# Optimization experiments

Measured on AMD Instinct MI355X. Metric: run time of the kernel, lower is better.

Reference implementation:

```python
import jax, jax.numpy as jnp
import numpy as np

SEG_LENS = [2048, 8192]
DIL_RATES = [1, 2]


def _dilated_attention(q, k, v, is_causal):
    # q,k,v: [b, n, h, d]
    b, n, h, d = q.shape
    ng = len(SEG_LENS)
    g = h // ng  # heads per group (even split)
    scale = 1.0 / np.sqrt(d).astype(np.float32)
    out = jnp.zeros_like(q)
    for i, (s, r) in enumerate(zip(SEG_LENS, DIL_RATES)):
        hs = i * g
        offset = i % r  # offset_idx % dilation_rate, as in _create_dilation_pattern
        idx = np.arange(offset, s, r)  # dilated positions within a segment, length m
        m = idx.shape[0]
        ns = n // s  # number of segments
        # reshape to segments then gather dilated positions: [b, ns, m, g, d]
        qg = q[:, :, hs:hs + g, :].reshape(b, ns, s, g, d)[:, :, idx]
        kg = k[:, :, hs:hs + g, :].reshape(b, ns, s, g, d)[:, :, idx]
        vg = v[:, :, hs:hs + g, :].reshape(b, ns, s, g, d)[:, :, idx]
        # segment-local attention over dilated tokens only (structured sparsity)
        scores = jnp.einsum('bsqhd,bskhd->bshqk', qg, kg) * scale
        if is_causal:
            cm = np.tril(np.ones((m, m), dtype=bool))  # idx is sorted -> causal in dilated order
            scores = jnp.where(cm, scores, -jnp.inf)
        attn = jax.nn.softmax(scores, axis=-1)
        og = jnp.einsum('bshqk,bskhd->bsqhd', attn, vg)  # [b, ns, m, g, d]
        # scatter back to full segment positions; non-dilated positions stay zero
        full = jnp.zeros((b, ns, s, g, d), q.dtype).at[:, :, idx].set(og)
        out = out.at[:, :, hs:hs + g, :].set(full.reshape(b, n, g, d))
    return out


def setup_inputs() -> dict:
    key = jax.random.key(0)
    k1, k2, k3 = jax.random.split(key, 3)
    shape = (1, 8192, 8, 64)
    q = jax.random.normal(k1, shape, dtype=jnp.float32)
    k = jax.random.normal(k2, shape, dtype=jnp.float32)
    v = jax.random.normal(k3, shape, dtype=jnp.float32)
    return {"q": q, "k": k, "v": v, "is_causal": 1}


def reference(q, k, v, is_causal):
    return _dilated_attention(q, k, v, bool(is_causal))
```

## Files before the change

### kernel.cpp

```cpp
#include <hip/hip_runtime.h>


#define LP 72

typedef __attribute__((ext_vector_type(8))) short bf16x8;
typedef __attribute__((ext_vector_type(4))) float f32x4;
typedef __attribute__((ext_vector_type(4))) unsigned u32x4;
typedef const unsigned int __attribute__((address_space(1)))* gp1;
typedef unsigned int __attribute__((address_space(3)))* lp3;

__device__ __forceinline__ unsigned short f2bf(float f) {
  unsigned u = __builtin_bit_cast(unsigned, f);
  u += 0x7fff + ((u >> 16) & 1);
  return (unsigned short)(u >> 16);
}

__device__ __forceinline__ int region_base(int head) {
  return (head < 4) ? head * 524288 : 2097152 + (head - 4) * 262144;
}

__device__ __forceinline__ void gl_lds16(const unsigned short* g, unsigned short* l) {
  __builtin_amdgcn_global_load_lds((gp1)g, (lp3)l, 16, 0, 0);
}

__global__ __launch_bounds__(256, 4)
void prep_kernel(const float* __restrict__ K, const float* __restrict__ V,
                 unsigned short* __restrict__ Kb, unsigned short* __restrict__ Vt) {
  __shared__ unsigned short sT[64][LP];
  const int bid = blockIdx.x;
  int head, pos0, rate, off;
  if (bid < 512) { head = bid >> 7; pos0 = (bid & 127) * 64; rate = 1; off = 0; }
  else { int b = bid - 512; head = 4 + (b >> 6); pos0 = (b & 63) * 64; rate = 2; off = 1; }
  const int rb = region_base(head);
  const int tid = threadIdx.x;
  const int row = tid >> 2, dg = tid & 3;
  const long tok = (long)(pos0 + row) * rate + off;

  {
    const float* kp = K + tok * 512 + head * 64 + dg * 16;
    unsigned short tmp[16];
    #pragma unroll
    for (int i = 0; i < 4; ++i) {
      float4 f = ((const float4*)kp)[i];
      tmp[i * 4 + 0] = f2bf(f.x); tmp[i * 4 + 1] = f2bf(f.y);
      tmp[i * 4 + 2] = f2bf(f.z); tmp[i * 4 + 3] = f2bf(f.w);
    }
    const int s = row & 7;
    unsigned short* dstrow = Kb + rb + (long)(pos0 + row) * 64;
    *(int4*)(dstrow + (((2 * dg)     ^ s) * 8)) = ((int4*)tmp)[0];
    *(int4*)(dstrow + (((2 * dg + 1) ^ s) * 8)) = ((int4*)tmp)[1];
  }

  {
    const float* vp = V + tok * 512 + head * 64 + dg * 16;
    #pragma unroll
    for (int i = 0; i < 4; ++i) {
      float4 f = ((const float4*)vp)[i];
      unsigned* p = (unsigned*)&sT[row][dg * 16 + i * 4];
      p[0] = (unsigned)f2bf(f.x) | ((unsigned)f2bf(f.y) << 16);
      p[1] = (unsigned)f2bf(f.z) | ((unsigned)f2bf(f.w) << 16);
    }
  }
  __syncthreads();

  {
    const int wv = tid >> 6, lane = tid & 63;
    unsigned pk[8];
    #pragma unroll
    for (int j = 0; j < 8; ++j) {
      unsigned lo = sT[wv * 16 + 2 * j][lane];
      unsigned hi = sT[wv * 16 + 2 * j + 1][lane];
      pk[j] = lo | (hi << 16);
    }
    int4 a = {(int)pk[0], (int)pk[1], (int)pk[2], (int)pk[3]};
    int4 b = {(int)pk[4], (int)pk[5], (int)pk[6], (int)pk[7]};
    const int dt = lane >> 4, l16p = lane & 15, h = wv >> 1;
    const int qa = (wv & 1) * 2, qb = qa + 1;
    unsigned short* dstc = Vt + rb + (long)pos0 * 64;
    *(int4*)(dstc + (dt * 2 + h) * 512 + (qa * 16 + l16p) * 8) = a;
    *(int4*)(dstc + (dt * 2 + h) * 512 + (qb * 16 + l16p) * 8) = b;
  }
}

__global__ __launch_bounds__(256, 2)
void attn_kernel(const float* __restrict__ Q, const unsigned short* __restrict__ Kb,
                 const unsigned short* __restrict__ Vt, const int* __restrict__ IC,
                 float* __restrict__ O, float* __restrict__ Slots) {
  __shared__ __attribute__((aligned(16))) unsigned short sK[2][4096];

  const int bid = blockIdx.x;
  int head, q0, seg0, mseg, rate, off, grp, chunk, slot;
  if (bid < 512) {
    int h4 = bid & 3;
    int u = bid >> 2;
    chunk = u >> 6;
    int t = 63 - (u & 63);
    head = 4 + h4; seg0 = 0; mseg = 4096;
    rate = 2; off = 1; grp = 1;
    q0 = t * 64;
    slot = (h4 * 64 + t) * 2 + chunk;
  } else {
    int cc = bid - 512;
    int job = (cc & 7) | ((cc >> 8) << 3);
    int tloc = (cc & 255) >> 3;
    head = job & 3;
    seg0 = (job >> 2) * 2048;
    q0 = seg0 + tloc * 64; mseg = 2048;
    rate = 1; off = 0; grp = 0; chunk = 0; slot = 0;
  }
  const int rb = region_base(head);
  const bool causal = (*IC) != 0;
  const int tid = threadIdx.x, wave = tid >> 6, lane = tid & 63;
  const int l16 = lane & 15, quad = lane >> 4;
  const int ch0 = ((quad ^ (l16 & 7)) * 8);
  const int ch1 = ch0 ^ 32;

  const int qloc = q0 - seg0;
  const int diagkb = qloc >> 6;
  const int nkb = causal ? diagkb + 1 : (mseg >> 6);
  const int klo = grp ? chunk * 32 : 0;
  const int khi = grp ? min(nkb, klo + 32) : nkb;
  if (klo >= khi) return;

  const float QSCALE = 0.18033688011112042f;
  bf16x8 aQ[2];
  {
    long tok = (long)(q0 + wave * 16 + l16) * rate + off;
    const float* qp = Q + tok * 512 + head * 64 + quad * 8;
    #pragma unroll
    for (int kc = 0; kc < 2; ++kc) {
      float4 f0 = ((const float4*)(qp + kc * 32))[0];
      float4 f1 = ((const float4*)(qp + kc * 32))[1];
      bf16x8 a;
      a[0] = (short)f2bf(f0.x * QSCALE); a[1] = (short)f2bf(f0.y * QSCALE);
      a[2] = (short)f2bf(f0.z * QSCALE); a[3] = (short)f2bf(f0.w * QSCALE);
      a[4] = (short)f2bf(f1.x * QSCALE); a[5] = (short)f2bf(f1.y * QSCALE);
      a[6] = (short)f2bf(f1.z * QSCALE); a[7] = (short)f2bf(f1.w * QSCALE);
      aQ[kc] = a;
    }
  }

  f32x4 oacc[4];
  float lsum = 0.f;
  #pragma unroll
  for (int dt = 0; dt < 4; ++dt) oacc[dt] = (f32x4){0.f, 0.f, 0.f, 0.f};

  const unsigned short* Ksrc = Kb + rb + (long)seg0 * 64;
  const unsigned short* Vsrc = Vt + rb + (long)seg0 * 64;

  const int o0 = wave * 1024;
  const int lo = lane * 8;
  const int qv = qloc + wave * 16 + l16;

  auto stage_k = [&](int x, int sl) {
    const unsigned short* kt = Ksrc + (long)x * 4096;
    gl_lds16(kt + o0 + lo,       &sK[sl][o0]);
    gl_lds16(kt + o0 + 512 + lo, &sK[sl][o0 + 512]);
  };

  struct PB { bf16x8 b0, b1; };
  auto qk_phase = [&](int kb, const unsigned short* kbuf) -> PB {
    f32x4 sc[4];
    #pragma unroll
    for (int c = 0; c < 4; ++c) {
      const unsigned short* krow = &kbuf[(c * 16 + l16) * 64];
      bf16x8 b0 = *(const bf16x8*)(krow + ch0);
      bf16x8 b1 = *(const bf16x8*)(krow + ch1);
      f32x4 z = (f32x4){0.f, 0.f, 0.f, 0.f};
      z = __builtin_amdgcn_mfma_f32_16x16x32_bf16(b0, aQ[0], z, 0, 0, 0);
      z = __builtin_amdgcn_mfma_f32_16x16x32_bf16(b1, aQ[1], z, 0, 0, 0);
      sc[c] = z;
    }

    float p[4][4];
    if (causal && (kb == diagkb)) {
      #pragma unroll
      for (int c = 0; c < 4; ++c)
        #pragma unroll
        for (int r = 0; r < 4; ++r) {
          float e = __builtin_amdgcn_exp2f(sc[c][r]);
          if (kb * 64 + c * 16 + quad * 4 + r > qv) e = 0.f;
          p[c][r] = e;
        }
    } else {
      #pragma unroll
      for (int c = 0; c < 4; ++c)
        #pragma unroll
        for (int r = 0; r < 4; ++r)
          p[c][r] = __builtin_amdgcn_exp2f(sc[c][r]);
    }

    lsum += (((p[0][0] + p[0][1]) + (p[0][2] + p[0][3])) +
             ((p[1][0] + p[1][1]) + (p[1][2] + p[1][3]))) +
            (((p[2][0] + p[2][1]) + (p[2][2] + p[2][3])) +
             ((p[3][0] + p[3][1]) + (p[3][2] + p[3][3])));

    unsigned W00, W01, W10, W11, W20, W21, W30, W31;
    asm("v_cvt_pk_bf16_f32 %0, %1, %2" : "=v"(W00) : "v"(p[0][0]), "v"(p[0][1]));
    asm("v_cvt_pk_bf16_f32 %0, %1, %2" : "=v"(W01) : "v"(p[0][2]), "v"(p[0][3]));
    asm("v_cvt_pk_bf16_f32 %0, %1, %2" : "=v"(W10) : "v"(p[1][0]), "v"(p[1][1]));
    asm("v_cvt_pk_bf16_f32 %0, %1, %2" : "=v"(W11) : "v"(p[1][2]), "v"(p[1][3]));
    asm("v_cvt_pk_bf16_f32 %0, %1, %2" : "=v"(W20) : "v"(p[2][0]), "v"(p[2][1]));
    asm("v_cvt_pk_bf16_f32 %0, %1, %2" : "=v"(W21) : "v"(p[2][2]), "v"(p[2][3]));
    asm("v_cvt_pk_bf16_f32 %0, %1, %2" : "=v"(W30) : "v"(p[3][0]), "v"(p[3][1]));
    asm("v_cvt_pk_bf16_f32 %0, %1, %2" : "=v"(W31) : "v"(p[3][2]), "v"(p[3][3]));

    unsigned R0 = W00, R2 = W10;
    asm("v_permlane32_swap_b32 %0, %1" : "+v"(R0), "+v"(R2));
    asm("v_permlane16_swap_b32 %0, %1" : "+v"(R0), "+v"(R2));
    unsigned R1 = W01, R3 = W11;
    asm("v_permlane32_swap_b32 %0, %1" : "+v"(R1), "+v"(R3));
    asm("v_permlane16_swap_b32 %0, %1" : "+v"(R1), "+v"(R3));
    unsigned R4 = W20, R6 = W30;
    asm("v_permlane32_swap_b32 %0, %1" : "+v"(R4), "+v"(R6));
    asm("v_permlane16_swap_b32 %0, %1" : "+v"(R4), "+v"(R6));
    unsigned R5 = W21, R7 = W31;
    asm("v_permlane32_swap_b32 %0, %1" : "+v"(R5), "+v"(R7));
    asm("v_permlane16_swap_b32 %0, %1" : "+v"(R5), "+v"(R7));
    u32x4 t0 = {R0, R1, R2, R3};
    u32x4 t1 = {R4, R5, R6, R7};
    PB pb;
    pb.b0 = __builtin_bit_cast(bf16x8, t0);
    pb.b1 = __builtin_bit_cast(bf16x8, t1);
    return pb;
  };

  stage_k(klo, 0);

  for (int kb = klo; kb < khi; ++kb) {
    const int cur = (kb - klo) & 1;
    __syncthreads();

    int4 vr[8];
    {
      const int4* vt = (const int4*)(Vsrc + (long)kb * 4096);
      #pragma unroll
      for (int c = 0; c < 8; ++c) vr[c] = vt[c * 64 + lane];
    }
    if (kb + 1 < khi) stage_k(kb + 1, cur ^ 1);

    PB pb = qk_phase(kb, &sK[cur][0]);

    #pragma unroll
    for (int dt = 0; dt < 4; ++dt) {
      bf16x8 v0 = __builtin_bit_cast(bf16x8, vr[dt * 2]);
      bf16x8 v1 = __builtin_bit_cast(bf16x8, vr[dt * 2 + 1]);
      oacc[dt] = __builtin_amdgcn_mfma_f32_16x16x32_bf16(v0, pb.b0, oacc[dt], 0, 0, 0);
      oacc[dt] = __builtin_amdgcn_mfma_f32_16x16x32_bf16(v1, pb.b1, oacc[dt], 0, 0, 0);
    }
  }

  float ltot = lsum;
  ltot += __shfl_xor(ltot, 16);
  ltot += __shfl_xor(ltot, 32);

  if (grp == 1) {
    float* S = Slots + (long)slot * 4160;
    const int qrow = wave * 16 + l16;
    #pragma unroll
    for (int dt = 0; dt < 4; ++dt)
      #pragma unroll
      for (int r = 0; r < 4; ++r)
        S[qrow * 64 + dt * 16 + quad * 4 + r] = oacc[dt][r];
    if (quad == 0) S[4096 + qrow] = ltot;
  } else {
    const int tq = q0 + wave * 16 + l16;
    const float inv = 1.0f / ltot;
    float* dst = O + (long)tq * 512 + head * 64 + quad * 4;
    #pragma unroll
    for (int dt = 0; dt < 4; ++dt)
      #pragma unroll
      for (int r = 0; r < 4; ++r)
        dst[dt * 16 + r] = oacc[dt][r] * inv;
  }
}

__global__ __launch_bounds__(256, 4)
void combine_kernel(const float* __restrict__ Slots, const int* __restrict__ IC,
                    float* __restrict__ O) {
  const int b = blockIdx.x;
  const int h4 = b >> 6, t = b & 63;
  const bool causal = (*IC) != 0;
  const int nkb = causal ? t + 1 : 64;
  const int nc = (nkb > 32) ? 2 : 1;
  const float* s0 = Slots + (long)((h4 * 64 + t) * 2) * 4160;
  const int tid = threadIdx.x;
  const int row = tid >> 2, dq = (tid & 3) * 16;

  float4 acc[4];
  const float4* p0 = (const float4*)(s0 + row * 64 + dq);
  #pragma unroll
  for (int i = 0; i < 4; ++i) acc[i] = p0[i];
  float l = s0[4096 + row];
  if (nc == 2) {
    const float* s1 = s0 + 4160;
    const float4* p1 = (const float4*)(s1 + row * 64 + dq);
    #pragma unroll
    for (int i = 0; i < 4; ++i) {
      float4 v = p1[i];
      acc[i].x += v.x; acc[i].y += v.y; acc[i].z += v.z; acc[i].w += v.w;
    }
    l += s1[4096 + row];
  }
  const float inv = 1.0f / l;
  const long tok = (long)(t * 64 + row) * 2 + 1;
  float* dst = O + tok * 512 + (4 + h4) * 64 + dq;
  #pragma unroll
  for (int i = 0; i < 4; ++i) {
    float4 o = {acc[i].x * inv, acc[i].y * inv, acc[i].z * inv, acc[i].w * inv};
    ((float4*)dst)[i] = o;
  }
  float* dste = O + (tok - 1) * 512 + (4 + h4) * 64 + dq;
  const float4 z = {0.f, 0.f, 0.f, 0.f};
  #pragma unroll
  for (int i = 0; i < 4; ++i) ((float4*)dste)[i] = z;
}

extern "C" void kernel_launch(void* const* d_in, const int* in_sizes, int n_in,
                              void* d_out, int out_size, void* d_ws, size_t ws_size,
                              hipStream_t stream) {
  const float* q = (const float*)d_in[0];
  const float* k = (const float*)d_in[1];
  const float* v = (const float*)d_in[2];
  const int* ic = (const int*)d_in[3];
  unsigned short* Kb = (unsigned short*)d_ws;
  unsigned short* Vt = Kb + 3145728;
  float* Slots = (float*)((char*)d_ws + 12582912);
  prep_kernel<<<dim3(768), dim3(256), 0, stream>>>(k, v, Kb, Vt);
  attn_kernel<<<dim3(1024), dim3(256), 0, stream>>>(q, Kb, Vt, ic, (float*)d_out, Slots);
  combine_kernel<<<dim3(256), dim3(256), 0, stream>>>(Slots, ic, (float*)d_out);
}
```

Baseline: 128.3 us.

## Split KV range into 16-block chunks for both head groups and interleave blocks

Attention work is now split along the key dimension into chunks of at most 16 key blocks for both the dilated and the dense head groups, so there are 2048 attention blocks instead of 1024. Even and odd block ids alternate between the two groups. Chunk 0 writes its unnormalized partial straight into the output plus a row-sum array. Later chunks write to slots, and a generalized combine kernel adds them and normalizes. Tiles that fit in a single chunk finish directly in the attention kernel. The aim is better load balance and shorter critical paths under causal masking, at the cost of more partial-result traffic and a larger combine pass.

```diff
diff --git a/kernel.cpp b/kernel.cpp
--- a/kernel.cpp
+++ b/kernel.cpp
@@ -85,28 +85,29 @@
 __global__ __launch_bounds__(256, 2)
 void attn_kernel(const float* __restrict__ Q, const unsigned short* __restrict__ Kb,
                  const unsigned short* __restrict__ Vt, const int* __restrict__ IC,
-                 float* __restrict__ O, float* __restrict__ Slots) {
+                 float* __restrict__ O, float* __restrict__ Slots,
+                 float* __restrict__ Lar) {
   __shared__ __attribute__((aligned(16))) unsigned short sK[2][4096];
 
   const int bid = blockIdx.x;
-  int head, q0, seg0, mseg, rate, off, grp, chunk, slot;
-  if (bid < 512) {
-    int h4 = bid & 3;
-    int u = bid >> 2;
-    chunk = u >> 6;
-    int t = 63 - (u & 63);
-    head = 4 + h4; seg0 = 0; mseg = 4096;
-    rate = 2; off = 1; grp = 1;
-    q0 = t * 64;
-    slot = (h4 * 64 + t) * 2 + chunk;
+  int head, q0, seg0, mseg, rate, off, grp, cnk, tloc, tileId;
+  if ((bid & 1) == 0) {
+    int idx = bid >> 1;
+    tloc = 63 - (idx >> 4);
+    cnk  = (idx >> 2) & 3;
+    int h4 = idx & 3;
+    head = 4 + h4; seg0 = 0; mseg = 4096; rate = 2; off = 1; grp = 1;
+    q0 = tloc * 64;
+    tileId = h4 * 64 + tloc;
   } else {
-    int cc = bid - 512;
-    int job = (cc & 7) | ((cc >> 8) << 3);
-    int tloc = (cc & 255) >> 3;
-    head = job & 3;
-    seg0 = (job >> 2) * 2048;
-    q0 = seg0 + tloc * 64; mseg = 2048;
-    rate = 1; off = 0; grp = 0; chunk = 0; slot = 0;
+    int idx = bid >> 1;
+    tloc = 31 - (idx >> 5);
+    cnk  = (idx >> 4) & 1;
+    int hs = idx & 15;
+    head = hs & 3; seg0 = (hs >> 2) * 2048;
+    mseg = 2048; rate = 1; off = 0; grp = 0;
+    q0 = seg0 + tloc * 64;
+    tileId = 256 + hs * 32 + tloc;
   }
   const int rb = region_base(head);
   const bool causal = (*IC) != 0;
@@ -118,9 +119,10 @@
   const int qloc = q0 - seg0;
   const int diagkb = qloc >> 6;
   const int nkb = causal ? diagkb + 1 : (mseg >> 6);
-  const int klo = grp ? chunk * 32 : 0;
-  const int khi = grp ? min(nkb, klo + 32) : nkb;
+  const int klo = cnk * 16;
+  const int khi = min(nkb, klo + 16);
   if (klo >= khi) return;
+  const int ncnk = (nkb + 15) >> 4;
 
   const float QSCALE = 0.18033688011112042f;
   bf16x8 aQ[2];
@@ -254,66 +256,103 @@
   ltot += __shfl_xor(ltot, 16);
   ltot += __shfl_xor(ltot, 32);
 
-  if (grp == 1) {
-    float* S = Slots + (long)slot * 4160;
-    const int qrow = wave * 16 + l16;
+  const int qrow = wave * 16 + l16;
+  if (ncnk == 1) {
+    const int tq = q0 + qrow;
+    const long tok = (long)tq * rate + off;
+    const float inv = 1.0f / ltot;
+    float* dst = O + tok * 512 + head * 64 + quad * 4;
+    #pragma unroll
+    for (int dt = 0; dt < 4; ++dt)
+      #pragma unroll
+      for (int r = 0; r < 4; ++r)
+        dst[dt * 16 + r] = oacc[dt][r] * inv;
+    if (grp) {
+      float* dste = O + (tok - 1) * 512 + head * 64 + quad * 4;
+      #pragma unroll
+      for (int dt = 0; dt < 4; ++dt)
+        #pragma unroll
+        for (int r = 0; r < 4; ++r)
+          dste[dt * 16 + r] = 0.f;
+    }
+  } else if (cnk == 0) {
+    const int tq = q0 + qrow;
+    const long tok = (long)tq * rate + off;
+    float* dst = O + tok * 512 + head * 64 + quad * 4;
+    #pragma unroll
+    for (int dt = 0; dt < 4; ++dt)
+      #pragma unroll
+      for (int r = 0; r < 4; ++r)
+        dst[dt * 16 + r] = oacc[dt][r];
+    if (quad == 0) Lar[tileId * 64 + qrow] = ltot;
+  } else {
+    const int slotId = grp ? (tileId * 3 + (cnk - 1)) : (tileId + 512);
+    float* S = Slots + (long)slotId * 4160;
     #pragma unroll
     for (int dt = 0; dt < 4; ++dt)
       #pragma unroll
       for (int r = 0; r < 4; ++r)
         S[qrow * 64 + dt * 16 + quad * 4 + r] = oacc[dt][r];
     if (quad == 0) S[4096 + qrow] = ltot;
+  }
+}
+
+__global__ __launch_bounds__(256, 4)
+void combine_kernel(const float* __restrict__ Slots, const float* __restrict__ Lar,
+                    const int* __restrict__ IC, float* __restrict__ O) {
+  const int b = blockIdx.x;
+  const bool causal = (*IC) != 0;
+  int grp, head, tloc, tileId, nkb;
+  int seg0 = 0;
+  if (b < 256) {
+    grp = 1; head = 4 + (b & 3); tloc = b >> 2;
+    tileId = (b & 3) * 64 + tloc;
+    nkb = causal ? tloc + 1 : 64;
   } else {
-    const int tq = q0 + wave * 16 + l16;
-    const float inv = 1.0f / ltot;
-    float* dst = O + (long)tq * 512 + head * 64 + quad * 4;
-    #pragma unroll
-    for (int dt = 0; dt < 4; ++dt)
-      #pragma unroll
-      for (int r = 0; r < 4; ++r)
-        dst[dt * 16 + r] = oacc[dt][r] * inv;
-  }
-}
-
-__global__ __launch_bounds__(256, 4)
-void combine_kernel(const float* __restrict__ Slots, const int* __restrict__ IC,
-                    float* __restrict__ O) {
-  const int b = blockIdx.x;
-  const int h4 = b >> 6, t = b & 63;
-  const bool causal = (*IC) != 0;
-  const int nkb = causal ? t + 1 : 64;
-  const int nc = (nkb > 32) ? 2 : 1;
-  const float* s0 = Slots + (long)((h4 * 64 + t) * 2) * 4160;
+    int u = b - 256;
+    grp = 0; int hs = u & 15; head = hs & 3; seg0 = (hs >> 2) * 2048;
+    tloc = u >> 4;
+    tileId = 256 + hs * 32 + tloc;
+    nkb = causal ? tloc + 1 : 32;
+  }
+  const int ncnk = (nkb + 15) >> 4;
+  if (ncnk < 2) return;
+
   const int tid = threadIdx.x;
   const int row = tid >> 2, dq = (tid & 3) * 16;
+  long tok;
+  if (grp) tok = (long)(tloc * 64 + row) * 2 + 1;
+  else     tok = (long)(seg0 + tloc * 64 + row);
+  float* dst = O + tok * 512 + head * 64 + dq;
 
   float4 acc[4];
-  const float4* p0 = (const float4*)(s0 + row * 64 + dq);
   #pragma unroll
-  for (int i = 0; i < 4; ++i) acc[i] = p0[i];
-  float l = s0[4096 + row];
-  if (nc == 2) {
-    const float* s1 = s0 + 4160;
-    const float4* p1 = (const float4*)(s1 + row * 64 + dq);
+  for (int i = 0; i < 4; ++i) acc[i] = ((const float4*)dst)[i];
+  float l = Lar[tileId * 64 + row];
+
+  for (int c = 1; c < ncnk; ++c) {
+    const int slotId = grp ? (tileId * 3 + (c - 1)) : (tileId + 512);
+    const float* S = Slots + (long)slotId * 4160;
+    const float4* p = (const float4*)(S + row * 64 + dq);
     #pragma unroll
     for (int i = 0; i < 4; ++i) {
-      float4 v = p1[i];
+      float4 v = p[i];
       acc[i].x += v.x; acc[i].y += v.y; acc[i].z += v.z; acc[i].w += v.w;
     }
-    l += s1[4096 + row];
+    l += S[4096 + row];
   }
   const float inv = 1.0f / l;
-  const long tok = (long)(t * 64 + row) * 2 + 1;
-  float* dst = O + tok * 512 + (4 + h4) * 64 + dq;
   #pragma unroll
   for (int i = 0; i < 4; ++i) {
     float4 o = {acc[i].x * inv, acc[i].y * inv, acc[i].z * inv, acc[i].w * inv};
     ((float4*)dst)[i] = o;
   }
-  float* dste = O + (tok - 1) * 512 + (4 + h4) * 64 + dq;
-  const float4 z = {0.f, 0.f, 0.f, 0.f};
-  #pragma unroll
-  for (int i = 0; i < 4; ++i) ((float4*)dste)[i] = z;
+  if (grp) {
+    float* dste = O + (tok - 1) * 512 + head * 64 + dq;
+    const float4 z = {0.f, 0.f, 0.f, 0.f};
+    #pragma unroll
+    for (int i = 0; i < 4; ++i) ((float4*)dste)[i] = z;
+  }
 }
 
 extern "C" void kernel_launch(void* const* d_in, const int* in_sizes, int n_in,
@@ -326,7 +365,8 @@
   unsigned short* Kb = (unsigned short*)d_ws;
   unsigned short* Vt = Kb + 3145728;
   float* Slots = (float*)((char*)d_ws + 12582912);
+  float* Lar = Slots + (long)1280 * 4160;
   prep_kernel<<<dim3(768), dim3(256), 0, stream>>>(k, v, Kb, Vt);
-  attn_kernel<<<dim3(1024), dim3(256), 0, stream>>>(q, Kb, Vt, ic, (float*)d_out, Slots);
-  combine_kernel<<<dim3(256), dim3(256), 0, stream>>>(Slots, ic, (float*)d_out);
-}
+  attn_kernel<<<dim3(2048), dim3(256), 0, stream>>>(q, Kb, Vt, ic, (float*)d_out, Slots, Lar);
+  combine_kernel<<<dim3(768), dim3(256), 0, stream>>>(Slots, Lar, ic, (float*)d_out);
+}
```

Measured after the change: 145.1 us. +13.1%, slower.

## Store K in MFMA fragment order and load directly to registers, drop LDS staging

Applied to the files above, without the earlier changes.

The prep kernel now writes K in the same fragment-major layout already used for V, so each lane's MFMA operand sits in contiguous 16-byte chunks. The attention kernel drops the double-buffered LDS staging of K, its global_load_lds calls and the per-iteration __syncthreads, and instead loads K and V straight from global memory into registers. This removes block-wide barriers and LDS traffic. In exchange each wave now fetches K itself with no prefetch of the next block, so load latency is less hidden, and register pressure rises.

```diff
diff --git a/kernel.cpp b/kernel.cpp
--- a/kernel.cpp
+++ b/kernel.cpp
@@ -6,8 +6,6 @@
 typedef __attribute__((ext_vector_type(8))) short bf16x8;
 typedef __attribute__((ext_vector_type(4))) float f32x4;
 typedef __attribute__((ext_vector_type(4))) unsigned u32x4;
-typedef const unsigned int __attribute__((address_space(1)))* gp1;
-typedef unsigned int __attribute__((address_space(3)))* lp3;
 
 __device__ __forceinline__ unsigned short f2bf(float f) {
   unsigned u = __builtin_bit_cast(unsigned, f);
@@ -17,10 +15,6 @@
 
 __device__ __forceinline__ int region_base(int head) {
   return (head < 4) ? head * 524288 : 2097152 + (head - 4) * 262144;
-}
-
-__device__ __forceinline__ void gl_lds16(const unsigned short* g, unsigned short* l) {
-  __builtin_amdgcn_global_load_lds((gp1)g, (lp3)l, 16, 0, 0);
 }
 
 __global__ __launch_bounds__(256, 4)
@@ -45,10 +39,11 @@
       tmp[i * 4 + 0] = f2bf(f.x); tmp[i * 4 + 1] = f2bf(f.y);
       tmp[i * 4 + 2] = f2bf(f.z); tmp[i * 4 + 3] = f2bf(f.w);
     }
-    const int s = row & 7;
-    unsigned short* dstrow = Kb + rb + (long)(pos0 + row) * 64;
-    *(int4*)(dstrow + (((2 * dg)     ^ s) * 8)) = ((int4*)tmp)[0];
-    *(int4*)(dstrow + (((2 * dg + 1) ^ s) * 8)) = ((int4*)tmp)[1];
+    const int c2 = (row >> 4) * 2 + (dg >> 1);
+    const int qp = (dg & 1) * 2;
+    unsigned short* dstc = Kb + rb + (long)pos0 * 64;
+    *(int4*)(dstc + c2 * 512 + ((qp    ) * 16 + (row & 15)) * 8) = ((int4*)tmp)[0];
+    *(int4*)(dstc + c2 * 512 + ((qp + 1) * 16 + (row & 15)) * 8) = ((int4*)tmp)[1];
   }
 
   {
@@ -86,8 +81,6 @@
 void attn_kernel(const float* __restrict__ Q, const unsigned short* __restrict__ Kb,
                  const unsigned short* __restrict__ Vt, const int* __restrict__ IC,
                  float* __restrict__ O, float* __restrict__ Slots) {
-  __shared__ __attribute__((aligned(16))) unsigned short sK[2][4096];
-
   const int bid = blockIdx.x;
   int head, q0, seg0, mseg, rate, off, grp, chunk, slot;
   if (bid < 512) {
@@ -112,8 +105,6 @@
   const bool causal = (*IC) != 0;
   const int tid = threadIdx.x, wave = tid >> 6, lane = tid & 63;
   const int l16 = lane & 15, quad = lane >> 4;
-  const int ch0 = ((quad ^ (l16 & 7)) * 8);
-  const int ch1 = ch0 ^ 32;
 
   const int qloc = q0 - seg0;
   const int diagkb = qloc >> 6;
@@ -147,25 +138,24 @@
 
   const unsigned short* Ksrc = Kb + rb + (long)seg0 * 64;
   const unsigned short* Vsrc = Vt + rb + (long)seg0 * 64;
-
-  const int o0 = wave * 1024;
-  const int lo = lane * 8;
   const int qv = qloc + wave * 16 + l16;
 
-  auto stage_k = [&](int x, int sl) {
-    const unsigned short* kt = Ksrc + (long)x * 4096;
-    gl_lds16(kt + o0 + lo,       &sK[sl][o0]);
-    gl_lds16(kt + o0 + 512 + lo, &sK[sl][o0 + 512]);
-  };
-
-  struct PB { bf16x8 b0, b1; };
-  auto qk_phase = [&](int kb, const unsigned short* kbuf) -> PB {
+  for (int kb = klo; kb < khi; ++kb) {
+    int4 kr[8], vr[8];
+    {
+      const int4* kt = (const int4*)(Ksrc + (long)kb * 4096);
+      #pragma unroll
+      for (int c = 0; c < 8; ++c) kr[c] = kt[c * 64 + lane];
+      const int4* vt = (const int4*)(Vsrc + (long)kb * 4096);
+      #pragma unroll
+      for (int c = 0; c < 8; ++c) vr[c] = vt[c * 64 + lane];
+    }
+
     f32x4 sc[4];
     #pragma unroll
     for (int c = 0; c < 4; ++c) {
-      const unsigned short* krow = &kbuf[(c * 16 + l16) * 64];
-      bf16x8 b0 = *(const bf16x8*)(krow + ch0);
-      bf16x8 b1 = *(const bf16x8*)(krow + ch1);
+      bf16x8 b0 = __builtin_bit_cast(bf16x8, kr[c * 2]);
+      bf16x8 b1 = __builtin_bit_cast(bf16x8, kr[c * 2 + 1]);
       f32x4 z = (f32x4){0.f, 0.f, 0.f, 0.f};
       z = __builtin_amdgcn_mfma_f32_16x16x32_bf16(b0, aQ[0], z, 0, 0, 0);
       z = __builtin_amdgcn_mfma_f32_16x16x32_bf16(b1, aQ[1], z, 0, 0, 0);
@@ -219,34 +209,15 @@
     asm("v_permlane16_swap_b32 %0, %1" : "+v"(R5), "+v"(R7));
     u32x4 t0 = {R0, R1, R2, R3};
     u32x4 t1 = {R4, R5, R6, R7};
-    PB pb;
-    pb.b0 = __builtin_bit_cast(bf16x8, t0);
-    pb.b1 = __builtin_bit_cast(bf16x8, t1);
-    return pb;
-  };
-
-  stage_k(klo, 0);
-
-  for (int kb = klo; kb < khi; ++kb) {
-    const int cur = (kb - klo) & 1;
-    __syncthreads();
-
-    int4 vr[8];
-    {
-      const int4* vt = (const int4*)(Vsrc + (long)kb * 4096);
-      #pragma unroll
-      for (int c = 0; c < 8; ++c) vr[c] = vt[c * 64 + lane];
-    }
-    if (kb + 1 < khi) stage_k(kb + 1, cur ^ 1);
-
-    PB pb = qk_phase(kb, &sK[cur][0]);
+    bf16x8 pB0 = __builtin_bit_cast(bf16x8, t0);
+    bf16x8 pB1 = __builtin_bit_cast(bf16x8, t1);
 
     #pragma unroll
     for (int dt = 0; dt < 4; ++dt) {
       bf16x8 v0 = __builtin_bit_cast(bf16x8, vr[dt * 2]);
       bf16x8 v1 = __builtin_bit_cast(bf16x8, vr[dt * 2 + 1]);
-      oacc[dt] = __builtin_amdgcn_mfma_f32_16x16x32_bf16(v0, pb.b0, oacc[dt], 0, 0, 0);
-      oacc[dt] = __builtin_amdgcn_mfma_f32_16x16x32_bf16(v1, pb.b1, oacc[dt], 0, 0, 0);
+      oacc[dt] = __builtin_amdgcn_mfma_f32_16x16x32_bf16(v0, pB0, oacc[dt], 0, 0, 0);
+      oacc[dt] = __builtin_amdgcn_mfma_f32_16x16x32_bf16(v1, pB1, oacc[dt], 0, 0, 0);
     }
   }
 
```

Result: slower. 133.0 us (+3.7%).

## Process two query sub-tiles per wave with 128-thread attention blocks

Applied to the files above, without the earlier changes.

The attention kernel now launches 2 waves per block instead of 4, and each wave handles two 16-row query sub-tiles (A and B) against the same K fragments and V registers. K LDS reads and V global loads are reused across twice as many query rows per wave, which halves the per-block V register loads and LDS K fetch traffic per query. In exchange, each wave holds double the accumulators and score registers, which raises register pressure and may lower occupancy. There are also fewer waves per block to hide latency.

```diff
diff --git a/kernel.cpp b/kernel.cpp
--- a/kernel.cpp
+++ b/kernel.cpp
@@ -82,7 +82,7 @@
   }
 }
 
-__global__ __launch_bounds__(256, 2)
+__global__ __launch_bounds__(128, 2)
 void attn_kernel(const float* __restrict__ Q, const unsigned short* __restrict__ Kb,
                  const unsigned short* __restrict__ Vt, const int* __restrict__ IC,
                  float* __restrict__ O, float* __restrict__ Slots) {
@@ -123,63 +123,61 @@
   if (klo >= khi) return;
 
   const float QSCALE = 0.18033688011112042f;
-  bf16x8 aQ[2];
+  bf16x8 aQA[2], aQB[2];
   {
-    long tok = (long)(q0 + wave * 16 + l16) * rate + off;
-    const float* qp = Q + tok * 512 + head * 64 + quad * 8;
-    #pragma unroll
-    for (int kc = 0; kc < 2; ++kc) {
-      float4 f0 = ((const float4*)(qp + kc * 32))[0];
-      float4 f1 = ((const float4*)(qp + kc * 32))[1];
-      bf16x8 a;
-      a[0] = (short)f2bf(f0.x * QSCALE); a[1] = (short)f2bf(f0.y * QSCALE);
-      a[2] = (short)f2bf(f0.z * QSCALE); a[3] = (short)f2bf(f0.w * QSCALE);
-      a[4] = (short)f2bf(f1.x * QSCALE); a[5] = (short)f2bf(f1.y * QSCALE);
-      a[6] = (short)f2bf(f1.z * QSCALE); a[7] = (short)f2bf(f1.w * QSCALE);
-      aQ[kc] = a;
-    }
-  }
-
-  f32x4 oacc[4];
-  float lsum = 0.f;
-  #pragma unroll
-  for (int dt = 0; dt < 4; ++dt) oacc[dt] = (f32x4){0.f, 0.f, 0.f, 0.f};
+    #pragma unroll
+    for (int st = 0; st < 2; ++st) {
+      long tok = (long)(q0 + st * 32 + wave * 16 + l16) * rate + off;
+      const float* qp = Q + tok * 512 + head * 64 + quad * 8;
+      #pragma unroll
+      for (int kc = 0; kc < 2; ++kc) {
+        float4 f0 = ((const float4*)(qp + kc * 32))[0];
+        float4 f1 = ((const float4*)(qp + kc * 32))[1];
+        bf16x8 a;
+        a[0] = (short)f2bf(f0.x * QSCALE); a[1] = (short)f2bf(f0.y * QSCALE);
+        a[2] = (short)f2bf(f0.z * QSCALE); a[3] = (short)f2bf(f0.w * QSCALE);
+        a[4] = (short)f2bf(f1.x * QSCALE); a[5] = (short)f2bf(f1.y * QSCALE);
+        a[6] = (short)f2bf(f1.z * QSCALE); a[7] = (short)f2bf(f1.w * QSCALE);
+        if (st == 0) aQA[kc] = a; else aQB[kc] = a;
+      }
+    }
+  }
+
+  f32x4 oaccA[4], oaccB[4];
+  float lsumA = 0.f, lsumB = 0.f;
+  #pragma unroll
+  for (int dt = 0; dt < 4; ++dt) {
+    oaccA[dt] = (f32x4){0.f, 0.f, 0.f, 0.f};
+    oaccB[dt] = (f32x4){0.f, 0.f, 0.f, 0.f};
+  }
 
   const unsigned short* Ksrc = Kb + rb + (long)seg0 * 64;
   const unsigned short* Vsrc = Vt + rb + (long)seg0 * 64;
 
-  const int o0 = wave * 1024;
+  const int o0 = wave * 2048;
   const int lo = lane * 8;
-  const int qv = qloc + wave * 16 + l16;
+  const int qvA = qloc + wave * 16 + l16;
+  const int qvB = qvA + 32;
 
   auto stage_k = [&](int x, int sl) {
     const unsigned short* kt = Ksrc + (long)x * 4096;
-    gl_lds16(kt + o0 + lo,       &sK[sl][o0]);
-    gl_lds16(kt + o0 + 512 + lo, &sK[sl][o0 + 512]);
+    gl_lds16(kt + o0 + lo,        &sK[sl][o0]);
+    gl_lds16(kt + o0 + 512 + lo,  &sK[sl][o0 + 512]);
+    gl_lds16(kt + o0 + 1024 + lo, &sK[sl][o0 + 1024]);
+    gl_lds16(kt + o0 + 1536 + lo, &sK[sl][o0 + 1536]);
   };
 
   struct PB { bf16x8 b0, b1; };
-  auto qk_phase = [&](int kb, const unsigned short* kbuf) -> PB {
-    f32x4 sc[4];
-    #pragma unroll
-    for (int c = 0; c < 4; ++c) {
-      const unsigned short* krow = &kbuf[(c * 16 + l16) * 64];
-      bf16x8 b0 = *(const bf16x8*)(krow + ch0);
-      bf16x8 b1 = *(const bf16x8*)(krow + ch1);
-      f32x4 z = (f32x4){0.f, 0.f, 0.f, 0.f};
-      z = __builtin_amdgcn_mfma_f32_16x16x32_bf16(b0, aQ[0], z, 0, 0, 0);
-      z = __builtin_amdgcn_mfma_f32_16x16x32_bf16(b1, aQ[1], z, 0, 0, 0);
-      sc[c] = z;
-    }
-
+  auto softmax_pack = [&](const f32x4* sc, int qvx, float& ls,
+                          bool needMask, int kb) -> PB {
     float p[4][4];
-    if (causal && (kb == diagkb)) {
+    if (needMask) {
       #pragma unroll
       for (int c = 0; c < 4; ++c)
         #pragma unroll
         for (int r = 0; r < 4; ++r) {
           float e = __builtin_amdgcn_exp2f(sc[c][r]);
-          if (kb * 64 + c * 16 + quad * 4 + r > qv) e = 0.f;
+          if (kb * 64 + c * 16 + quad * 4 + r > qvx) e = 0.f;
           p[c][r] = e;
         }
     } else {
@@ -190,10 +188,10 @@
           p[c][r] = __builtin_amdgcn_exp2f(sc[c][r]);
     }
 
-    lsum += (((p[0][0] + p[0][1]) + (p[0][2] + p[0][3])) +
-             ((p[1][0] + p[1][1]) + (p[1][2] + p[1][3]))) +
-            (((p[2][0] + p[2][1]) + (p[2][2] + p[2][3])) +
-             ((p[3][0] + p[3][1]) + (p[3][2] + p[3][3])));
+    ls += (((p[0][0] + p[0][1]) + (p[0][2] + p[0][3])) +
+           ((p[1][0] + p[1][1]) + (p[1][2] + p[1][3]))) +
+          (((p[2][0] + p[2][1]) + (p[2][2] + p[2][3])) +
+           ((p[3][0] + p[3][1]) + (p[3][2] + p[3][3])));
 
     unsigned W00, W01, W10, W11, W20, W21, W30, W31;
     asm("v_cvt_pk_bf16_f32 %0, %1, %2" : "=v"(W00) : "v"(p[0][0]), "v"(p[0][1]));
@@ -239,39 +237,67 @@
     }
     if (kb + 1 < khi) stage_k(kb + 1, cur ^ 1);
 
-    PB pb = qk_phase(kb, &sK[cur][0]);
+    f32x4 scA[4], scB[4];
+    #pragma unroll
+    for (int c = 0; c < 4; ++c) {
+      const unsigned short* krow = &sK[cur][(c * 16 + l16) * 64];
+      bf16x8 b0 = *(const bf16x8*)(krow + ch0);
+      bf16x8 b1 = *(const bf16x8*)(krow + ch1);
+      f32x4 zA = (f32x4){0.f, 0.f, 0.f, 0.f};
+      zA = __builtin_amdgcn_mfma_f32_16x16x32_bf16(b0, aQA[0], zA, 0, 0, 0);
+      zA = __builtin_amdgcn_mfma_f32_16x16x32_bf16(b1, aQA[1], zA, 0, 0, 0);
+      scA[c] = zA;
+      f32x4 zB = (f32x4){0.f, 0.f, 0.f, 0.f};
+      zB = __builtin_amdgcn_mfma_f32_16x16x32_bf16(b0, aQB[0], zB, 0, 0, 0);
+      zB = __builtin_amdgcn_mfma_f32_16x16x32_bf16(b1, aQB[1], zB, 0, 0, 0);
+      scB[c] = zB;
+    }
+
+    const bool needMask = causal && (kb == diagkb);
+    PB pbA = softmax_pack(scA, qvA, lsumA, needMask, kb);
+    PB pbB = softmax_pack(scB, qvB, lsumB, needMask, kb);
 
     #pragma unroll
     for (int dt = 0; dt < 4; ++dt) {
       bf16x8 v0 = __builtin_bit_cast(bf16x8, vr[dt * 2]);
       bf16x8 v1 = __builtin_bit_cast(bf16x8, vr[dt * 2 + 1]);
-      oacc[dt] = __builtin_amdgcn_mfma_f32_16x16x32_bf16(v0, pb.b0, oacc[dt], 0, 0, 0);
-      oacc[dt] = __builtin_amdgcn_mfma_f32_16x16x32_bf16(v1, pb.b1, oacc[dt], 0, 0, 0);
-    }
-  }
-
-  float ltot = lsum;
-  ltot += __shfl_xor(ltot, 16);
-  ltot += __shfl_xor(ltot, 32);
-
-  if (grp == 1) {
-    float* S = Slots + (long)slot * 4160;
-    const int qrow = wave * 16 + l16;
-    #pragma unroll
-    for (int dt = 0; dt < 4; ++dt)
-      #pragma unroll
-      for (int r = 0; r < 4; ++r)
-        S[qrow * 64 + dt * 16 + quad * 4 + r] = oacc[dt][r];
-    if (quad == 0) S[4096 + qrow] = ltot;
-  } else {
-    const int tq = q0 + wave * 16 + l16;
-    const float inv = 1.0f / ltot;
-    float* dst = O + (long)tq * 512 + head * 64 + quad * 4;
-    #pragma unroll
-    for (int dt = 0; dt < 4; ++dt)
-      #pragma unroll
-      for (int r = 0; r < 4; ++r)
-        dst[dt * 16 + r] = oacc[dt][r] * inv;
+      oaccA[dt] = __builtin_amdgcn_mfma_f32_16x16x32_bf16(v0, pbA.b0, oaccA[dt], 0, 0, 0);
+      oaccA[dt] = __builtin_amdgcn_mfma_f32_16x16x32_bf16(v1, pbA.b1, oaccA[dt], 0, 0, 0);
+      oaccB[dt] = __builtin_amdgcn_mfma_f32_16x16x32_bf16(v0, pbB.b0, oaccB[dt], 0, 0, 0);
+      oaccB[dt] = __builtin_amdgcn_mfma_f32_16x16x32_bf16(v1, pbB.b1, oaccB[dt], 0, 0, 0);
+    }
+  }
+
+  float ltotA = lsumA;
+  ltotA += __shfl_xor(ltotA, 16);
+  ltotA += __shfl_xor(ltotA, 32);
+  float ltotB = lsumB;
+  ltotB += __shfl_xor(ltotB, 16);
+  ltotB += __shfl_xor(ltotB, 32);
+
+  #pragma unroll
+  for (int st = 0; st < 2; ++st) {
+    const int qrow = st * 32 + wave * 16 + l16;
+    const float ltot = st ? ltotB : ltotA;
+    const f32x4* oacc = st ? oaccB : oaccA;
+    if (grp == 1) {
+      float* S = Slots + (long)slot * 4160;
+      #pragma unroll
+      for (int dt = 0; dt < 4; ++dt)
+        #pragma unroll
+        for (int r = 0; r < 4; ++r)
+          S[qrow * 64 + dt * 16 + quad * 4 + r] = oacc[dt][r];
+      if (quad == 0) S[4096 + qrow] = ltot;
+    } else {
+      const int tq = q0 + qrow;
+      const float inv = 1.0f / ltot;
+      float* dst = O + (long)tq * 512 + head * 64 + quad * 4;
+      #pragma unroll
+      for (int dt = 0; dt < 4; ++dt)
+        #pragma unroll
+        for (int r = 0; r < 4; ++r)
+          dst[dt * 16 + r] = oacc[dt][r] * inv;
+    }
   }
 }
 
@@ -327,6 +353,6 @@
   unsigned short* Vt = Kb + 3145728;
   float* Slots = (float*)((char*)d_ws + 12582912);
   prep_kernel<<<dim3(768), dim3(256), 0, stream>>>(k, v, Kb, Vt);
-  attn_kernel<<<dim3(1024), dim3(256), 0, stream>>>(q, Kb, Vt, ic, (float*)d_out, Slots);
+  attn_kernel<<<dim3(1024), dim3(128), 0, stream>>>(q, Kb, Vt, ic, (float*)d_out, Slots);
   combine_kernel<<<dim3(256), dim3(256), 0, stream>>>(Slots, ic, (float*)d_out);
 }
```

Result: slower. 137.4 us (+7.1%).
